# Kernel optimization log

Measured on AMD Instinct MI355X. Metric: run time of the kernel, lower is better.

The kernel has to match this reference:

```python
import jax, jax.numpy as jnp
import numpy as np

N = 50000      # nodes
E = 800000     # edges per relation/layer
L = 2          # GCN layer_num
D = 128        # input_dim == output_dim


def setup_inputs() -> dict:
    key = jax.random.key(0)
    ks = jax.random.split(key, 11)
    x = jax.random.normal(ks[0], (N, D), jnp.float32)
    hidden = jax.random.normal(ks[1], (N, D), jnp.float32)
    adj_src = jax.random.randint(ks[2], (L, E), 0, N)
    adj_dst = jax.random.randint(ks[3], (L, E), 0, N)
    adj_w = jax.random.uniform(ks[4], (L, E), jnp.float32)
    std = 1.0 / np.sqrt(D)  # reset_parameters: uniform(-std, std)
    def u(k, shape):
        return jax.random.uniform(k, shape, jnp.float32, -std, std)
    gcn_W = u(ks[5], (L, D, D))
    gcn_b = u(ks[6], (L, D))
    x2h_W = u(ks[7], (D, 3 * D))
    x2h_b = u(ks[8], (3 * D,))
    h2h_W = u(ks[9], (D, 3 * D))
    h2h_b = u(ks[10], (3 * D,))
    return dict(x=x, hidden=hidden, adj_src=adj_src, adj_dst=adj_dst, adj_w=adj_w,
                gcn_W=gcn_W, gcn_b=gcn_b, x2h_W=x2h_W, x2h_b=x2h_b,
                h2h_W=h2h_W, h2h_b=h2h_b)


def reference(x, hidden, adj_src, adj_dst, adj_w, gcn_W, gcn_b,
              x2h_W, x2h_b, h2h_W, h2h_b):
    # MRGCN: layer_num GCN layers, layer l uses relation l's sparse adjacency.
    h = x
    for l in range(L):
        support = h @ gcn_W[l]                              # [N, D]
        msg = support[adj_src[l]] * adj_w[l][:, None]       # [E, D] irregular gather
        agg = jax.ops.segment_sum(msg, adj_dst[l], num_segments=N)  # spmm scatter-add
        h = jax.nn.relu(agg + gcn_b[l])
    # GRU gate chain (dropout=0 / eval mode)
    gate_x = h @ x2h_W + x2h_b                              # [N, 3D]
    gate_h = hidden @ h2h_W + h2h_b                         # [N, 3D]
    i_r, i_i, i_n = jnp.split(gate_x, 3, axis=1)
    h_r, h_i, h_n = jnp.split(gate_h, 3, axis=1)
    resetgate = jax.nn.sigmoid(i_r + h_r)
    inputgate = jax.nn.sigmoid(i_i + h_i)
    newgate = jnp.tanh(i_n + resetgate * h_n)
    hy = newgate + inputgate * (hidden - newgate)
    return hy
```

## Files before the change

### kernel.cpp

```cpp
#include <hip/hip_runtime.h>

#define D 128
#define RPW 8
#define ROWS_PB 32

typedef __attribute__((ext_vector_type(8))) short short8;
typedef __attribute__((ext_vector_type(4))) float f32x4;

static __device__ __forceinline__ ushort f2bf(float f) {
    unsigned u = __float_as_uint(f);
    unsigned r = (u + 0x7fffu + ((u >> 16) & 1u)) >> 16;
    return (ushort)r;
}

static __device__ __forceinline__ void gemm_compute(const float* sw, float (*sh)[D],
                                                    ushort* __restrict__ outb,
                                                    int N, int row0, int tid) {
    int wid = tid >> 6, lane = tid & 63;
    int rb = wid * RPW;
    float acc0[RPW], acc1[RPW];
#pragma unroll
    for (int r = 0; r < RPW; ++r) { acc0[r] = 0.f; acc1[r] = 0.f; }
    for (int k = 0; k < D; k += 4) {
        float w0[4], w1[4];
#pragma unroll
        for (int kk = 0; kk < 4; ++kk) {
            w0[kk] = sw[(k + kk) * D + lane];
            w1[kk] = sw[(k + kk) * D + lane + 64];
        }
#pragma unroll
        for (int r = 0; r < RPW; ++r) {
            float4 a4 = *(const float4*)&sh[rb + r][k];
            acc0[r] = fmaf(a4.x, w0[0], acc0[r]); acc1[r] = fmaf(a4.x, w1[0], acc1[r]);
            acc0[r] = fmaf(a4.y, w0[1], acc0[r]); acc1[r] = fmaf(a4.y, w1[1], acc1[r]);
            acc0[r] = fmaf(a4.z, w0[2], acc0[r]); acc1[r] = fmaf(a4.z, w1[2], acc1[r]);
            acc0[r] = fmaf(a4.w, w0[3], acc0[r]); acc1[r] = fmaf(a4.w, w1[3], acc1[r]);
        }
    }
#pragma unroll
    for (int r = 0; r < RPW; ++r) {
        int row = row0 + rb + r;
        if (row < N) {
            outb[(size_t)row * D + lane] = f2bf(acc0[r]);
            outb[(size_t)row * D + lane + 64] = f2bf(acc1[r]);
        }
    }
}

static __device__ __forceinline__ void gemm_body(float* sw, float (*sh)[D],
                                                 const float* __restrict__ in,
                                                 const float* __restrict__ W,
                                                 ushort* __restrict__ outb,
                                                 int N, int bid, int tid) {
    int row0 = bid * ROWS_PB;
    for (int j = tid; j < D * D / 4; j += 256)
        ((float4*)sw)[j] = ((const float4*)W)[j];
    for (int i = tid; i < ROWS_PB * (D / 4); i += 256) {
        int r = i >> 5, c4 = i & 31;
        int row = row0 + r;
        float4 v = (row < N) ? ((const float4*)(in + (size_t)row * D))[c4]
                             : make_float4(0.f, 0.f, 0.f, 0.f);
        ((float4*)sh)[i] = v;
    }
    __syncthreads();
    gemm_compute(sw, sh, outb, N, row0, tid);
}

__global__ __launch_bounds__(256) void fused_sgc(const float* __restrict__ x,
                                                 const float* __restrict__ W0,
                                                 ushort* __restrict__ Abf, int N,
                                                 const int* __restrict__ adj_dst,
                                                 int* __restrict__ counts,
                                                 ushort* __restrict__ pl, int E2,
                                                 int E, int GB,
                                                 const float* __restrict__ Wx,
                                                 const float* __restrict__ Wh,
                                                 ushort* __restrict__ wxt,
                                                 ushort* __restrict__ wht) {
    __shared__ float sw[D * D];
    __shared__ float sh[ROWS_PB][D];
    int bid = blockIdx.x, tid = threadIdx.x;
    int five = GB * 5;
    if (bid < five) {
        int g = bid / 5, j = bid - g * 5;
        if (j == 0) {
            gemm_body(sw, sh, x, W0, Abf, N, g, tid);
        } else {
            int i = (g * 4 + j - 1) * 256 + tid;
            if (i < E2) {
                int off = (i >= E) ? N : 0;
                pl[i] = (ushort)atomicAdd(&counts[off + adj_dst[i]], 1);
            }
        }
    } else {
        int i = (bid - five) * 256 + tid;
        if (i < 384 * 128) {
            int c = i >> 7, k = i & 127;
            wxt[i] = f2bf(Wx[(size_t)k * 384 + c]);
            wht[i] = f2bf(Wh[(size_t)k * 384 + c]);
        }
    }
}

__global__ __launch_bounds__(256) void gemm_rowbatch_bfin(const ushort* __restrict__ in,
                                                          const float* __restrict__ W,
                                                          ushort* __restrict__ outb, int N) {
    __shared__ float sw[D * D];
    __shared__ float sh[ROWS_PB][D];
    int tid = threadIdx.x;
    int row0 = blockIdx.x * ROWS_PB;
    for (int j = tid; j < D * D / 4; j += 256)
        ((float4*)sw)[j] = ((const float4*)W)[j];
    for (int i = tid; i < ROWS_PB * (D / 4); i += 256) {
        int r = i >> 5, c4 = i & 31;
        int row = row0 + r;
        float4 v;
        if (row < N) {
            uint2 u = ((const uint2*)(in + (size_t)row * D))[c4];
            v.x = __uint_as_float(u.x << 16);
            v.y = __uint_as_float(u.x & 0xffff0000u);
            v.z = __uint_as_float(u.y << 16);
            v.w = __uint_as_float(u.y & 0xffff0000u);
        } else {
            v = make_float4(0.f, 0.f, 0.f, 0.f);
        }
        ((float4*)sh)[i] = v;
    }
    __syncthreads();
    gemm_compute(sw, sh, outb, N, row0, tid);
}

__global__ void zero_int4(int4* __restrict__ p, int n4) {
    int i = blockIdx.x * blockDim.x + threadIdx.x;
    if (i < n4) p[i] = make_int4(0, 0, 0, 0);
}

__global__ __launch_bounds__(256) void scan_partial(const int4* __restrict__ counts4,
                                                    int* __restrict__ bsum) {
    int b = blockIdx.x, t = threadIdx.x;
    int4 c0 = counts4[(size_t)b * 512 + t * 2];
    int4 c1 = counts4[(size_t)b * 512 + t * 2 + 1];
    int s = c0.x + c0.y + c0.z + c0.w + c1.x + c1.y + c1.z + c1.w;
#pragma unroll
    for (int d = 1; d < 64; d <<= 1) s += __shfl_xor(s, d);
    __shared__ int ws[4];
    if ((t & 63) == 0) ws[t >> 6] = s;
    __syncthreads();
    if (t == 0) bsum[b] = ws[0] + ws[1] + ws[2] + ws[3];
}

__global__ void scan_base(const int* __restrict__ bsum, int* __restrict__ bbase, int nb) {
    int lane = threadIdx.x;
    int run = 0;
    for (int c = 0; c < nb; c += 64) {
        int v = (c + lane < nb) ? bsum[c + lane] : 0;
        int inc = v;
#pragma unroll
        for (int d = 1; d < 64; d <<= 1) {
            int y = __shfl_up(inc, d);
            if (lane >= d) inc += y;
        }
        if (c + lane < nb) bbase[c + lane] = run + inc - v;
        run += __shfl(inc, 63);
    }
}

__global__ __launch_bounds__(256) void scan_apply(const int4* __restrict__ counts4,
                                                  const int* __restrict__ bbase,
                                                  int4* __restrict__ off4) {
    __shared__ int ts[256];
    int b = blockIdx.x, t = threadIdx.x;
    int4 c0 = counts4[(size_t)b * 512 + t * 2];
    int4 c1 = counts4[(size_t)b * 512 + t * 2 + 1];
    int s = c0.x + c0.y + c0.z + c0.w + c1.x + c1.y + c1.z + c1.w;
    ts[t] = s;
    __syncthreads();
    for (int d = 1; d < 256; d <<= 1) {
        int x = ts[t];
        int y = (t >= d) ? ts[t - d] : 0;
        __syncthreads();
        ts[t] = x + y;
        __syncthreads();
    }
    int base = bbase[b] + ((t == 0) ? 0 : ts[t - 1]);
    int4 o0, o1;
    o0.x = base;
    o0.y = o0.x + c0.x;
    o0.z = o0.y + c0.y;
    o0.w = o0.z + c0.z;
    o1.x = o0.w + c0.w;
    o1.y = o1.x + c1.x;
    o1.z = o1.y + c1.y;
    o1.w = o1.z + c1.z;
    off4[(size_t)b * 512 + t * 2] = o0;
    off4[(size_t)b * 512 + t * 2 + 1] = o1;
}

__global__ void place2_kernel(const int* __restrict__ src, const int* __restrict__ dst,
                              const float* __restrict__ w,
                              const int* __restrict__ offsets2,
                              const ushort* __restrict__ pl,
                              int2* __restrict__ srcw0, int2* __restrict__ srcw1,
                              int E, int E2, int N) {
    int i = blockIdx.x * blockDim.x + threadIdx.x;
    if (i >= E2) return;
    int l1 = i >= E;
    int node = dst[i];
    int p = offsets2[(l1 ? N : 0) + node] - (l1 ? E : 0) + (int)pl[i];
    int2 v = make_int2(src[i], __float_as_int(w[i]));
    (l1 ? srcw1 : srcw0)[p] = v;
}

static __device__ __forceinline__ void gather_row(const ushort* __restrict__ base,
                                                  const int2* __restrict__ srcw,
                                                  int lo, int hi,
                                                  float& ax, float& ay) {
    ax = 0.f; ay = 0.f;
    int j = lo;
    for (; j + 8 <= hi; j += 8) {
        int2 s[8];
        uint v[8];
#pragma unroll
        for (int u = 0; u < 8; ++u) s[u] = srcw[j + u];
#pragma unroll
        for (int u = 0; u < 8; ++u)
            v[u] = *(const uint*)(base + ((size_t)s[u].x << 7));
#pragma unroll
        for (int u = 0; u < 8; ++u) {
            float wt = __int_as_float(s[u].y);
            ax = fmaf(wt, __uint_as_float(v[u] << 16), ax);
            ay = fmaf(wt, __uint_as_float(v[u] & 0xffff0000u), ay);
        }
    }
    for (; j < hi; ++j) {
        int2 sw = srcw[j];
        float wt = __int_as_float(sw.y);
        uint v = *(const uint*)(base + ((size_t)sw.x << 7));
        ax = fmaf(wt, __uint_as_float(v << 16), ax);
        ay = fmaf(wt, __uint_as_float(v & 0xffff0000u), ay);
    }
}

__global__ void gather_nodes_bf(const ushort* __restrict__ supb,
                                const int2* __restrict__ srcw,
                                const int* __restrict__ offsets, int sub,
                                const float* __restrict__ bias,
                                ushort* __restrict__ outb, int N) {
    int node = (blockIdx.x * blockDim.x + threadIdx.x) >> 6;
    int lane = threadIdx.x & 63;
    if (node >= N) return;
    int lo = offsets[node] - sub, hi = offsets[node + 1] - sub;
    int c = lane * 2;
    float ax, ay;
    gather_row(supb + c, srcw, lo, hi, ax, ay);
    float2 bi = *(const float2*)(bias + c);
    uint pk = ((uint)f2bf(fmaxf(ay + bi.y, 0.f)) << 16) | (uint)f2bf(fmaxf(ax + bi.x, 0.f));
    *(uint*)(outb + (size_t)node * D + c) = pk;
}

#define QROWS 192
#define KPAD 136
__global__ __launch_bounds__(256) void gru_mfma_lds(const ushort* __restrict__ hb,
                                                    const float* __restrict__ hidden,
                                                    const ushort* __restrict__ wxt,
                                                    const ushort* __restrict__ wht,
                                                    const float* __restrict__ bx,
                                                    const float* __restrict__ bh,
                                                    float* __restrict__ out, int N) {
    __shared__ ushort lw[QROWS * KPAD];
    int tid = threadIdx.x;
    int wid = tid >> 6, lane = tid & 63;
    int nstripes = (N + 15) >> 4;
    int stripe = blockIdx.x * 4 + wid;
    bool live = stripe < nstripes;
    int row0 = stripe * 16;
    int lr = lane & 15;
    int lk = (lane >> 4) * 8;

    short8 Ah[4], Ad[4];
    if (live) {
        const ushort* hrow = hb + (size_t)(row0 + lr) * D + lk;
        const float* drow = hidden + (size_t)(row0 + lr) * D + lk;
#pragma unroll
        for (int ks = 0; ks < 4; ++ks) {
            Ah[ks] = *(const short8*)(hrow + ks * 32);
            float4 c0 = *(const float4*)(drow + ks * 32);
            float4 c1 = *(const float4*)(drow + ks * 32 + 4);
            short8 vc;
            vc[0] = f2bf(c0.x); vc[1] = f2bf(c0.y); vc[2] = f2bf(c0.z); vc[3] = f2bf(c0.w);
            vc[4] = f2bf(c1.x); vc[5] = f2bf(c1.y); vc[6] = f2bf(c1.z); vc[7] = f2bf(c1.w);
            Ad[ks] = vc;
        }
    }
    int orow = row0 + (lane >> 4) * 4;

    for (int q = 0; q < 4; ++q) {
        if (q) __syncthreads();
        for (int j = tid; j < QROWS * 16; j += 256) {
            int chunk = j & 15;
            int row = j >> 4;
            int mat = row >= 96;
            int r = row - (mat ? 96 : 0);
            int g = r >> 5;
            int c = r & 31;
            const ushort* srcp = (mat ? wht : wxt)
                               + ((size_t)(g * 128 + q * 32 + c) << 7) + (chunk << 3);
            *(short8*)&lw[row * KPAD + chunk * 8] = *(const short8*)srcp;
        }
        __syncthreads();
        if (!live) continue;

#pragma unroll
        for (int mt = 0; mt < 2; ++mt) {
            int cl = mt * 16 + lr;
            const ushort* bx0 = lw + (0 * 32 + cl) * KPAD + lk;
            const ushort* bx1 = lw + (1 * 32 + cl) * KPAD + lk;
            const ushort* bx2 = lw + (2 * 32 + cl) * KPAD + lk;
            const ushort* bh0 = lw + ((96 + 0 * 32) + cl) * KPAD + lk;
            const ushort* bh1 = lw + ((96 + 1 * 32) + cl) * KPAD + lk;
            const ushort* bh2 = lw + ((96 + 2 * 32) + cl) * KPAD + lk;
            f32x4 ax0{}, ax1{}, ax2{}, ah0{}, ah1{}, ah2{};
#pragma unroll
            for (int ks = 0; ks < 4; ++ks) {
                short8 w0 = *(const short8*)(bx0 + ks * 32);
                short8 w1 = *(const short8*)(bx1 + ks * 32);
                short8 w2 = *(const short8*)(bx2 + ks * 32);
                short8 v0 = *(const short8*)(bh0 + ks * 32);
                short8 v1 = *(const short8*)(bh1 + ks * 32);
                short8 v2 = *(const short8*)(bh2 + ks * 32);
                ax0 = __builtin_amdgcn_mfma_f32_16x16x32_bf16(Ah[ks], w0, ax0, 0, 0, 0);
                ax1 = __builtin_amdgcn_mfma_f32_16x16x32_bf16(Ah[ks], w1, ax1, 0, 0, 0);
                ax2 = __builtin_amdgcn_mfma_f32_16x16x32_bf16(Ah[ks], w2, ax2, 0, 0, 0);
                ah0 = __builtin_amdgcn_mfma_f32_16x16x32_bf16(Ad[ks], v0, ah0, 0, 0, 0);
                ah1 = __builtin_amdgcn_mfma_f32_16x16x32_bf16(Ad[ks], v1, ah1, 0, 0, 0);
                ah2 = __builtin_amdgcn_mfma_f32_16x16x32_bf16(Ad[ks], v2, ah2, 0, 0, 0);
            }
            int col = q * 32 + mt * 16 + lr;
            float bxr = bx[col], bxi = bx[col + 128], bxn = bx[col + 256];
            float bhr = bh[col], bhi = bh[col + 128], bhn = bh[col + 256];
#pragma unroll
            for (int r = 0; r < 4; ++r) {
                int row = orow + r;
                if (row < N) {
                    float ir = ax0[r] + bxr, hr = ah0[r] + bhr;
                    float ii = ax1[r] + bxi, hi = ah1[r] + bhi;
                    float in_ = ax2[r] + bxn, hn = ah2[r] + bhn;
                    float rg = 1.f / (1.f + __expf(-(ir + hr)));
                    float ig = 1.f / (1.f + __expf(-(ii + hi)));
                    float nx = in_ + rg * hn;
                    float ng = 1.f - 2.f / (__expf(2.f * nx) + 1.f);
                    float hv = hidden[(size_t)row * D + col];
                    out[(size_t)row * D + col] = ng + ig * (hv - ng);
                }
            }
        }
    }
}

extern "C" void kernel_launch(void* const* d_in, const int* in_sizes, int n_in,
                              void* d_out, int out_size, void* d_ws, size_t ws_size,
                              hipStream_t stream) {
    const float* x      = (const float*)d_in[0];
    const float* hidden = (const float*)d_in[1];
    const int*   adj_src = (const int*)d_in[2];
    const int*   adj_dst = (const int*)d_in[3];
    const float* adj_w   = (const float*)d_in[4];
    const float* gcn_W   = (const float*)d_in[5];
    const float* gcn_b   = (const float*)d_in[6];
    const float* x2h_W   = (const float*)d_in[7];
    const float* x2h_b   = (const float*)d_in[8];
    const float* h2h_W   = (const float*)d_in[9];
    const float* h2h_b   = (const float*)d_in[10];
    float* out = (float*)d_out;

    const int L = 2;
    const int N = in_sizes[0] / D;
    const int E = in_sizes[2] / L;
    const size_t nd = (size_t)N * D;

    const int twoN   = 2 * N;
    const int NB     = (twoN + 2047) / 2048;
    const int padded = NB * 2048;

    char* ws = (char*)d_ws;
    ushort* P       = (ushort*)ws;                ws += nd * 2;
    ushort* Q       = (ushort*)ws;                ws += nd * 2;
    int*   counts2  = (int*)ws;                   ws += (size_t)padded * 4;
    int*   offsets2 = (int*)ws;                   ws += ((size_t)padded + 64) * 4;
    int*   bsum     = (int*)ws;                   ws += ((size_t)NB + 64) * 4;
    int*   bbase    = (int*)ws;                   ws += ((size_t)NB + 64) * 4;
    int2*  srcw0    = (int2*)ws;                  ws += (size_t)E * 8;
    int2*  srcw1    = (int2*)ws;                  ws += (size_t)E * 8;
    ushort* pl      = (ushort*)ws;                ws += (size_t)2 * E * 2;
    ushort* wxt     = (ushort*)ws;                ws += (size_t)384 * 128 * 2;
    ushort* wht     = (ushort*)ws;                ws += (size_t)384 * 128 * 2;

    dim3 blk(256);
    int batch_blocks = (N + ROWS_PB - 1) / ROWS_PB;
    int gat_blocks   = (N + 3) / 4;
    int e2_blocks    = (2 * E + 255) / 256;
    int zero_blocks  = (padded / 4 + 255) / 256;
    int convw_blocks = (384 * 128 + 255) / 256;
    int nstripes     = (N + 15) / 16;
    int gru_blocks   = (nstripes + 3) / 4;

    zero_int4<<<zero_blocks, blk, 0, stream>>>((int4*)counts2, padded / 4);
    fused_sgc<<<batch_blocks * 5 + convw_blocks, blk, 0, stream>>>(
        x, gcn_W, P, N, adj_dst, counts2, pl, 2 * E, E, batch_blocks,
        x2h_W, h2h_W, wxt, wht);
    scan_partial<<<NB, blk, 0, stream>>>((const int4*)counts2, bsum);
    scan_base<<<1, 64, 0, stream>>>(bsum, bbase, NB);
    scan_apply<<<NB, blk, 0, stream>>>((const int4*)counts2, bbase, (int4*)offsets2);
    place2_kernel<<<e2_blocks, blk, 0, stream>>>(adj_src, adj_dst, adj_w, offsets2, pl,
                                                 srcw0, srcw1, E, 2 * E, N);
    gather_nodes_bf<<<gat_blocks, blk, 0, stream>>>(P, srcw0, offsets2, 0,
                                                    gcn_b, Q, N);
    gemm_rowbatch_bfin<<<batch_blocks, blk, 0, stream>>>(Q, gcn_W + (size_t)D * D,
                                                         P, N);
    gather_nodes_bf<<<gat_blocks, blk, 0, stream>>>(P, srcw1, offsets2 + N, E,
                                                    gcn_b + D, Q, N);
    gru_mfma_lds<<<gru_blocks, blk, 0, stream>>>(Q, hidden, wxt, wht, x2h_b, h2h_b,
                                                 out, N);
}
```

Measured before the change: 306.9 us.

## Split CSR build per relation and overlap relation-1 setup with layer-0 work

The two relations' CSR construction is split instead of being done together. Relation 0's counting is fused with the first GEMM. Relation 1's counting is fused with relation 0's placement, and relation 1's placement is fused with the layer-0 gather. The aim is to hide relation-1 preprocessing behind layer-0 compute and shrink the work on the critical path. In exchange it adds a second scan sequence (three more kernel launches) and makes the fused kernels more heterogeneous.

```diff
diff --git a/kernel.cpp b/kernel.cpp
--- a/kernel.cpp
+++ b/kernel.cpp
@@ -66,40 +66,132 @@
     gemm_compute(sw, sh, outb, N, row0, tid);
 }
 
-__global__ __launch_bounds__(256) void fused_sgc(const float* __restrict__ x,
+__global__ __launch_bounds__(256) void fused_gs0(const float* __restrict__ x,
                                                  const float* __restrict__ W0,
-                                                 ushort* __restrict__ Abf, int N,
-                                                 const int* __restrict__ adj_dst,
-                                                 int* __restrict__ counts,
-                                                 ushort* __restrict__ pl, int E2,
-                                                 int E, int GB,
+                                                 ushort* __restrict__ P, int N,
+                                                 const int* __restrict__ dst0,
+                                                 int* __restrict__ counts0,
+                                                 ushort* __restrict__ pl0, int E,
                                                  const float* __restrict__ Wx,
                                                  const float* __restrict__ Wh,
                                                  ushort* __restrict__ wxt,
-                                                 ushort* __restrict__ wht) {
+                                                 ushort* __restrict__ wht, int GB) {
     __shared__ float sw[D * D];
     __shared__ float sh[ROWS_PB][D];
     int bid = blockIdx.x, tid = threadIdx.x;
-    int five = GB * 5;
-    if (bid < five) {
-        int g = bid / 5, j = bid - g * 5;
+    int three = GB * 3;
+    if (bid < three) {
+        int g = bid / 3, j = bid - g * 3;
         if (j == 0) {
-            gemm_body(sw, sh, x, W0, Abf, N, g, tid);
+            gemm_body(sw, sh, x, W0, P, N, g, tid);
         } else {
-            int i = (g * 4 + j - 1) * 256 + tid;
-            if (i < E2) {
-                int off = (i >= E) ? N : 0;
-                pl[i] = (ushort)atomicAdd(&counts[off + adj_dst[i]], 1);
-            }
+            int i = (g * 2 + (j - 1)) * 256 + tid;
+            if (i < E)
+                pl0[i] = (ushort)atomicAdd(&counts0[dst0[i]], 1);
         }
     } else {
-        int i = (bid - five) * 256 + tid;
+        int i = (bid - three) * 256 + tid;
         if (i < 384 * 128) {
             int c = i >> 7, k = i & 127;
             wxt[i] = f2bf(Wx[(size_t)k * 384 + c]);
             wht[i] = f2bf(Wh[(size_t)k * 384 + c]);
         }
     }
+}
+
+__global__ void fused_ps1(const int* __restrict__ src0, const int* __restrict__ dst0,
+                          const float* __restrict__ w0,
+                          const int* __restrict__ offsets0,
+                          const ushort* __restrict__ pl0, int2* __restrict__ srcw0,
+                          const int* __restrict__ dst1, int* __restrict__ counts1,
+                          ushort* __restrict__ pl1, int E) {
+    int bid = blockIdx.x, tid = threadIdx.x;
+    int g = bid >> 1;
+    int i = g * 256 + tid;
+    if (i >= E) return;
+    if ((bid & 1) == 0) {
+        int p = offsets0[dst0[i]] + (int)pl0[i];
+        srcw0[p] = make_int2(src0[i], __float_as_int(w0[i]));
+    } else {
+        pl1[i] = (ushort)atomicAdd(&counts1[dst1[i]], 1);
+    }
+}
+
+static __device__ __forceinline__ void gather_row(const ushort* __restrict__ base,
+                                                  const int2* __restrict__ srcw,
+                                                  int lo, int hi,
+                                                  float& ax, float& ay) {
+    ax = 0.f; ay = 0.f;
+    int j = lo;
+    for (; j + 8 <= hi; j += 8) {
+        int2 s[8];
+        uint v[8];
+#pragma unroll
+        for (int u = 0; u < 8; ++u) s[u] = srcw[j + u];
+#pragma unroll
+        for (int u = 0; u < 8; ++u)
+            v[u] = *(const uint*)(base + ((size_t)s[u].x << 7));
+#pragma unroll
+        for (int u = 0; u < 8; ++u) {
+            float wt = __int_as_float(s[u].y);
+            ax = fmaf(wt, __uint_as_float(v[u] << 16), ax);
+            ay = fmaf(wt, __uint_as_float(v[u] & 0xffff0000u), ay);
+        }
+    }
+    for (; j < hi; ++j) {
+        int2 sw = srcw[j];
+        float wt = __int_as_float(sw.y);
+        uint v = *(const uint*)(base + ((size_t)sw.x << 7));
+        ax = fmaf(wt, __uint_as_float(v << 16), ax);
+        ay = fmaf(wt, __uint_as_float(v & 0xffff0000u), ay);
+    }
+}
+
+static __device__ __forceinline__ void gather_node_body(const ushort* __restrict__ supb,
+                                                        const int2* __restrict__ srcw,
+                                                        const int* __restrict__ offsets,
+                                                        const float* __restrict__ bias,
+                                                        ushort* __restrict__ outb,
+                                                        int node, int lane, int N) {
+    if (node >= N) return;
+    int lo = offsets[node], hi = offsets[node + 1];
+    int c = lane * 2;
+    float ax, ay;
+    gather_row(supb + c, srcw, lo, hi, ax, ay);
+    float2 bi = *(const float2*)(bias + c);
+    uint pk = ((uint)f2bf(fmaxf(ay + bi.y, 0.f)) << 16) | (uint)f2bf(fmaxf(ax + bi.x, 0.f));
+    *(uint*)(outb + (size_t)node * D + c) = pk;
+}
+
+__global__ void fused_gp1(const ushort* __restrict__ P, const int2* __restrict__ srcw0,
+                          const int* __restrict__ offsets0,
+                          const float* __restrict__ b0, ushort* __restrict__ Q, int N,
+                          const int* __restrict__ src1, const int* __restrict__ dst1,
+                          const float* __restrict__ w1,
+                          const int* __restrict__ offsets1,
+                          const ushort* __restrict__ pl1,
+                          int2* __restrict__ srcw1, int E) {
+    int bid = blockIdx.x, tid = threadIdx.x;
+    int g = bid / 5, j = bid - g * 5;
+    if (j < 4) {
+        int node = (g * 4 + j) * 4 + (tid >> 6);
+        gather_node_body(P, srcw0, offsets0, b0, Q, node, tid & 63, N);
+    } else {
+        int e = g * 256 + tid;
+        if (e < E) {
+            int p = offsets1[dst1[e]] + (int)pl1[e];
+            srcw1[p] = make_int2(src1[e], __float_as_int(w1[e]));
+        }
+    }
+}
+
+__global__ void gather_nodes_bf(const ushort* __restrict__ supb,
+                                const int2* __restrict__ srcw,
+                                const int* __restrict__ offsets,
+                                const float* __restrict__ bias,
+                                ushort* __restrict__ outb, int N) {
+    int node = (blockIdx.x * blockDim.x + threadIdx.x) >> 6;
+    gather_node_body(supb, srcw, offsets, bias, outb, node, threadIdx.x & 63, N);
 }
 
 __global__ __launch_bounds__(256) void gemm_rowbatch_bfin(const ushort* __restrict__ in,
@@ -196,68 +288,6 @@
     off4[(size_t)b * 512 + t * 2 + 1] = o1;
 }
 
-__global__ void place2_kernel(const int* __restrict__ src, const int* __restrict__ dst,
-                              const float* __restrict__ w,
-                              const int* __restrict__ offsets2,
-                              const ushort* __restrict__ pl,
-                              int2* __restrict__ srcw0, int2* __restrict__ srcw1,
-                              int E, int E2, int N) {
-    int i = blockIdx.x * blockDim.x + threadIdx.x;
-    if (i >= E2) return;
-    int l1 = i >= E;
-    int node = dst[i];
-    int p = offsets2[(l1 ? N : 0) + node] - (l1 ? E : 0) + (int)pl[i];
-    int2 v = make_int2(src[i], __float_as_int(w[i]));
-    (l1 ? srcw1 : srcw0)[p] = v;
-}
-
-static __device__ __forceinline__ void gather_row(const ushort* __restrict__ base,
-                                                  const int2* __restrict__ srcw,
-                                                  int lo, int hi,
-                                                  float& ax, float& ay) {
-    ax = 0.f; ay = 0.f;
-    int j = lo;
-    for (; j + 8 <= hi; j += 8) {
-        int2 s[8];
-        uint v[8];
-#pragma unroll
-        for (int u = 0; u < 8; ++u) s[u] = srcw[j + u];
-#pragma unroll
-        for (int u = 0; u < 8; ++u)
-            v[u] = *(const uint*)(base + ((size_t)s[u].x << 7));
-#pragma unroll
-        for (int u = 0; u < 8; ++u) {
-            float wt = __int_as_float(s[u].y);
-            ax = fmaf(wt, __uint_as_float(v[u] << 16), ax);
-            ay = fmaf(wt, __uint_as_float(v[u] & 0xffff0000u), ay);
-        }
-    }
-    for (; j < hi; ++j) {
-        int2 sw = srcw[j];
-        float wt = __int_as_float(sw.y);
-        uint v = *(const uint*)(base + ((size_t)sw.x << 7));
-        ax = fmaf(wt, __uint_as_float(v << 16), ax);
-        ay = fmaf(wt, __uint_as_float(v & 0xffff0000u), ay);
-    }
-}
-
-__global__ void gather_nodes_bf(const ushort* __restrict__ supb,
-                                const int2* __restrict__ srcw,
-                                const int* __restrict__ offsets, int sub,
-                                const float* __restrict__ bias,
-                                ushort* __restrict__ outb, int N) {
-    int node = (blockIdx.x * blockDim.x + threadIdx.x) >> 6;
-    int lane = threadIdx.x & 63;
-    if (node >= N) return;
-    int lo = offsets[node] - sub, hi = offsets[node + 1] - sub;
-    int c = lane * 2;
-    float ax, ay;
-    gather_row(supb + c, srcw, lo, hi, ax, ay);
-    float2 bi = *(const float2*)(bias + c);
-    uint pk = ((uint)f2bf(fmaxf(ay + bi.y, 0.f)) << 16) | (uint)f2bf(fmaxf(ax + bi.x, 0.f));
-    *(uint*)(outb + (size_t)node * D + c) = pk;
-}
-
 #define QROWS 192
 #define KPAD 136
 __global__ __launch_bounds__(256) void gru_mfma_lds(const ushort* __restrict__ hb,
@@ -378,47 +408,61 @@
     const int E = in_sizes[2] / L;
     const size_t nd = (size_t)N * D;
 
-    const int twoN   = 2 * N;
-    const int NB     = (twoN + 2047) / 2048;
-    const int padded = NB * 2048;
+    const int NBH     = (N + 2047) / 2048;
+    const int paddedH = NBH * 2048;
 
     char* ws = (char*)d_ws;
     ushort* P       = (ushort*)ws;                ws += nd * 2;
     ushort* Q       = (ushort*)ws;                ws += nd * 2;
-    int*   counts2  = (int*)ws;                   ws += (size_t)padded * 4;
-    int*   offsets2 = (int*)ws;                   ws += ((size_t)padded + 64) * 4;
-    int*   bsum     = (int*)ws;                   ws += ((size_t)NB + 64) * 4;
-    int*   bbase    = (int*)ws;                   ws += ((size_t)NB + 64) * 4;
+    int*   counts2  = (int*)ws;                   ws += (size_t)2 * paddedH * 4;
+    int*   offsets2 = (int*)ws;                   ws += ((size_t)2 * paddedH + 64) * 4;
+    int*   bsum     = (int*)ws;                   ws += ((size_t)NBH + 64) * 4;
+    int*   bbase    = (int*)ws;                   ws += ((size_t)NBH + 64) * 4;
     int2*  srcw0    = (int2*)ws;                  ws += (size_t)E * 8;
     int2*  srcw1    = (int2*)ws;                  ws += (size_t)E * 8;
     ushort* pl      = (ushort*)ws;                ws += (size_t)2 * E * 2;
     ushort* wxt     = (ushort*)ws;                ws += (size_t)384 * 128 * 2;
     ushort* wht     = (ushort*)ws;                ws += (size_t)384 * 128 * 2;
 
+    int*   counts0  = counts2;
+    int*   counts1  = counts2 + paddedH;
+    int*   offsets0 = offsets2;
+    int*   offsets1 = offsets2 + paddedH;
+    ushort* pl0 = pl;
+    ushort* pl1 = pl + E;
+
+    const int* dst0 = adj_dst;
+    const int* dst1 = adj_dst + E;
+    const int* src0 = adj_src;
+    const int* src1 = adj_src + E;
+    const float* w0 = adj_w;
+    const float* w1 = adj_w + E;
+
     dim3 blk(256);
     int batch_blocks = (N + ROWS_PB - 1) / ROWS_PB;
     int gat_blocks   = (N + 3) / 4;
-    int e2_blocks    = (2 * E + 255) / 256;
-    int zero_blocks  = (padded / 4 + 255) / 256;
+    int edge_blocks  = (E + 255) / 256;
+    int zero_blocks  = (2 * paddedH / 4 + 255) / 256;
     int convw_blocks = (384 * 128 + 255) / 256;
     int nstripes     = (N + 15) / 16;
     int gru_blocks   = (nstripes + 3) / 4;
 
-    zero_int4<<<zero_blocks, blk, 0, stream>>>((int4*)counts2, padded / 4);
-    fused_sgc<<<batch_blocks * 5 + convw_blocks, blk, 0, stream>>>(
-        x, gcn_W, P, N, adj_dst, counts2, pl, 2 * E, E, batch_blocks,
-        x2h_W, h2h_W, wxt, wht);
-    scan_partial<<<NB, blk, 0, stream>>>((const int4*)counts2, bsum);
-    scan_base<<<1, 64, 0, stream>>>(bsum, bbase, NB);
-    scan_apply<<<NB, blk, 0, stream>>>((const int4*)counts2, bbase, (int4*)offsets2);
-    place2_kernel<<<e2_blocks, blk, 0, stream>>>(adj_src, adj_dst, adj_w, offsets2, pl,
-                                                 srcw0, srcw1, E, 2 * E, N);
-    gather_nodes_bf<<<gat_blocks, blk, 0, stream>>>(P, srcw0, offsets2, 0,
-                                                    gcn_b, Q, N);
-    gemm_rowbatch_bfin<<<batch_blocks, blk, 0, stream>>>(Q, gcn_W + (size_t)D * D,
-                                                         P, N);
-    gather_nodes_bf<<<gat_blocks, blk, 0, stream>>>(P, srcw1, offsets2 + N, E,
-                                                    gcn_b + D, Q, N);
+    zero_int4<<<zero_blocks, blk, 0, stream>>>((int4*)counts2, 2 * paddedH / 4);
+    fused_gs0<<<batch_blocks * 3 + convw_blocks, blk, 0, stream>>>(
+        x, gcn_W, P, N, dst0, counts0, pl0, E, x2h_W, h2h_W, wxt, wht, batch_blocks);
+    scan_partial<<<NBH, blk, 0, stream>>>((const int4*)counts0, bsum);
+    scan_base<<<1, 64, 0, stream>>>(bsum, bbase, NBH);
+    scan_apply<<<NBH, blk, 0, stream>>>((const int4*)counts0, bbase, (int4*)offsets0);
+    fused_ps1<<<edge_blocks * 2, blk, 0, stream>>>(src0, dst0, w0, offsets0, pl0, srcw0,
+                                                   dst1, counts1, pl1, E);
+    scan_partial<<<NBH, blk, 0, stream>>>((const int4*)counts1, bsum);
+    scan_base<<<1, 64, 0, stream>>>(bsum, bbase, NBH);
+    scan_apply<<<NBH, blk, 0, stream>>>((const int4*)counts1, bbase, (int4*)offsets1);
+    fused_gp1<<<edge_blocks * 5, blk, 0, stream>>>(P, srcw0, offsets0, gcn_b, Q, N,
+                                                   src1, dst1, w1, offsets1, pl1,
+                                                   srcw1, E);
+    gemm_rowbatch_bfin<<<batch_blocks, blk, 0, stream>>>(Q, gcn_W + (size_t)D * D, P, N);
+    gather_nodes_bf<<<gat_blocks, blk, 0, stream>>>(P, srcw1, offsets1, gcn_b + D, Q, N);
     gru_mfma_lds<<<gru_blocks, blk, 0, stream>>>(Q, hidden, wxt, wht, x2h_b, h2h_b,
                                                  out, N);
 }
```

Result: slower. 323.5 us (+5.4%).
